# Optimization experiments

Measured on AMD Instinct MI355X. Metric: run time of the kernel, lower is better.

Reference implementation:

```python
import jax, jax.numpy as jnp
import numpy as np

N, E, D_IN, D_H, D_OUT = 100000, 1600000, 128, 128, 47
BN_EPS = 1e-5


def setup_inputs() -> dict:
    key = jax.random.key(0)
    ks = jax.random.split(key, 12)
    x = jax.random.normal(ks[0], (N, D_IN), dtype=jnp.float32)
    edge_index = jax.random.randint(ks[1], (2, E), 0, N, dtype=jnp.int64)
    s = 1.0 / np.sqrt(D_H)
    return {
        "x": x,
        "edge_index": edge_index,
        "W1": jax.random.normal(ks[2], (D_IN, D_H), dtype=jnp.float32) * s,
        "b1": jnp.zeros((D_H,), dtype=jnp.float32),
        "gamma": jax.random.uniform(ks[3], (D_H,), dtype=jnp.float32, minval=0.5, maxval=1.5),
        "beta": jax.random.normal(ks[4], (D_H,), dtype=jnp.float32) * 0.1,
        "mean": jax.random.normal(ks[5], (D_H,), dtype=jnp.float32) * 0.1,
        "var": jax.random.uniform(ks[6], (D_H,), dtype=jnp.float32, minval=0.5, maxval=1.5),
        "W2": jax.random.normal(ks[7], (D_H, D_H), dtype=jnp.float32) * s,
        "b2": jnp.zeros((D_H,), dtype=jnp.float32),
        "Wf": jax.random.normal(ks[8], (D_H, D_OUT), dtype=jnp.float32) * s,
        "bf": jnp.zeros((D_OUT,), dtype=jnp.float32),
    }


def gcn_conv(x, src, dst, W, b, n):
    # x' = x @ W, then symmetric-normalized aggregation with self-loops (PyG GCNConv).
    h = x @ W
    loops = jnp.arange(n, dtype=src.dtype)
    s = jnp.concatenate([src, loops])
    d = jnp.concatenate([dst, loops])
    deg = jax.ops.segment_sum(jnp.ones_like(d, dtype=h.dtype), d, num_segments=n)
    dinv = jnp.where(deg > 0, jax.lax.rsqrt(deg), 0.0)
    norm = dinv[s] * dinv[d]                      # [E+N]
    msg = h[s] * norm[:, None]                    # [E+N, D] gather
    out = jax.ops.segment_sum(msg, d, num_segments=n)  # scatter-add
    return out + b


def reference(x, edge_index, W1, b1, gamma, beta, mean, var, W2, b2, Wf, bf):
    n = x.shape[0]
    src, dst = edge_index[0], edge_index[1]
    # layer 1: GCNConv -> BatchNorm (eval) -> ReLU -> dropout (identity in eval)
    h1 = gcn_conv(x, src, dst, W1, b1, n)
    h1 = (h1 - mean) * jax.lax.rsqrt(var + BN_EPS) * gamma + beta
    h1 = jax.nn.relu(h1)
    # layer 2 (last conv, no BN/act)
    h2 = gcn_conv(h1, src, dst, W2, b2, n)
    # JumpingKnowledge max over layer outputs
    jk = jnp.maximum(h1, h2)
    logits = jk @ Wf + bf
    return jax.nn.log_softmax(logits, axis=1)
```

## Files before the change

kernel.cpp:

```cpp
#include <hip/hip_runtime.h>
#include <math.h>

#define DH 128
#define DOUT 47
#define BN_EPS 1e-5f

typedef __attribute__((ext_vector_type(8))) short short8;
typedef __attribute__((ext_vector_type(4))) float float4v;

__device__ __forceinline__ unsigned bf16_rne(float f) {
    unsigned u = __float_as_uint(f);
    return (u + 0x7fffu + ((u >> 16) & 1u)) >> 16;
}
__device__ __forceinline__ unsigned pack_bf2(float a, float b) {
    return (bf16_rne(a) & 0xffffu) | (bf16_rne(b) << 16);
}
__device__ __forceinline__ float2 unpack_bf2(unsigned u) {
    return make_float2(__uint_as_float(u << 16),
                       __uint_as_float(u & 0xffff0000u));
}


__global__ void zero_int_k(int* __restrict__ p, int n) {
    int i = blockIdx.x * 256 + threadIdx.x;
    if (i < n) p[i] = 0;
}

__global__ __launch_bounds__(256) void scan1_k(const int* __restrict__ counts,
                                               int* __restrict__ offsets,
                                               int* __restrict__ blocksums, int n) {
    __shared__ int sd[256];
    int tid = threadIdx.x;
    int base = blockIdx.x * 1024 + tid * 4;
    int v0 = (base + 0 < n) ? ((counts[base + 0] + 7) & ~7) : 0;
    int v1 = (base + 1 < n) ? ((counts[base + 1] + 7) & ~7) : 0;
    int v2 = (base + 2 < n) ? ((counts[base + 2] + 7) & ~7) : 0;
    int v3 = (base + 3 < n) ? ((counts[base + 3] + 7) & ~7) : 0;
    int tsum = v0 + v1 + v2 + v3;
    sd[tid] = tsum;
    __syncthreads();
    for (int off = 1; off < 256; off <<= 1) {
        int x = (tid >= off) ? sd[tid - off] : 0;
        __syncthreads();
        sd[tid] += x;
        __syncthreads();
    }
    if (tid == 255) blocksums[blockIdx.x] = sd[255];
    int run = sd[tid] - tsum;
    if (base + 0 < n) offsets[base + 0] = run;  run += v0;
    if (base + 1 < n) offsets[base + 1] = run;  run += v1;
    if (base + 2 < n) offsets[base + 2] = run;  run += v2;
    if (base + 3 < n) offsets[base + 3] = run;
}

__global__ __launch_bounds__(128) void scan2_k(int* __restrict__ blocksums, int nb) {
    __shared__ int sd[128];
    int tid = threadIdx.x;
    int v = (tid < nb) ? blocksums[tid] : 0;
    sd[tid] = v;
    __syncthreads();
    for (int off = 1; off < 128; off <<= 1) {
        int x = (tid >= off) ? sd[tid - off] : 0;
        __syncthreads();
        sd[tid] += x;
        __syncthreads();
    }
    if (tid < nb) blocksums[tid] = sd[tid] - v;
}

__global__ void finalize_k(int* __restrict__ offsets, int* __restrict__ cursor,
                           float* __restrict__ dinv, const int* __restrict__ counts,
                           const int* __restrict__ blocksums,
                           int2* __restrict__ ew, int n) {
    int i = blockIdx.x * 256 + threadIdx.x;
    if (i >= n) return;
    int o = offsets[i] + blocksums[i >> 10];
    offsets[i] = o;
    cursor[i] = o;
    int c = counts[i];
    dinv[i] = rsqrtf((float)(c + 1));
    int cP = (c + 7) & ~7;
    int2 z; z.x = 0; z.y = 0;
    for (int j = o + c; j < o + cP; ++j) ew[j] = z;
}

__global__ void fill_k(const int* __restrict__ src, const int* __restrict__ dst,
                       const float* __restrict__ dinv, int* __restrict__ cursor,
                       int2* __restrict__ ew, int e, int n) {
    int i = blockIdx.x * 256 + threadIdx.x;
    int stride = gridDim.x * 256;
    for (; i < e; i += stride) {
        int d = dst[i];
        if ((unsigned)d < (unsigned)n) {
            int s = src[i];
            int pos = atomicAdd(&cursor[d], 1);
            int2 rec;
            rec.x = s;
            rec.y = __float_as_int(dinv[s] * dinv[d]);
            ew[pos] = rec;
        }
    }
}

__global__ __launch_bounds__(256) void wprep_k(const float* __restrict__ W1,
                                               const float* __restrict__ W2,
                                               unsigned* __restrict__ W1b,
                                               unsigned* __restrict__ W2b) {
    const float* W = blockIdx.x ? W2 : W1;
    unsigned* Wb = blockIdx.x ? W2b : W1b;
    int tid = threadIdx.x;
    for (int p = tid; p < 128 * 32; p += 256) {
        int n = p >> 5;
        int k0 = (p & 31) << 2;
        float f0 = W[(size_t)(k0 + 0) * 128 + n];
        float f1 = W[(size_t)(k0 + 1) * 128 + n];
        float f2 = W[(size_t)(k0 + 2) * 128 + n];
        float f3 = W[(size_t)(k0 + 3) * 128 + n];
        uint2 v;
        v.x = pack_bf2(f0, f1);
        v.y = pack_bf2(f2, f3);
        *(uint2*)(Wb + (size_t)n * 64 + (k0 >> 1)) = v;
    }
}

#define COUNT_BLOCKS 2048

__device__ __forceinline__ void gemm_mfma_body(const float* __restrict__ A,
                                               const unsigned* __restrict__ Wb,
                                               unsigned* __restrict__ Cb, int M,
                                               int blk) {
    __shared__ ushort Bl[128 * 136];
    int tid = threadIdx.x;
    {
        unsigned* Bu = (unsigned*)Bl;
        for (int q = tid; q < 128 * 16; q += 256) {
            int row = q >> 4;
            int c = (q & 15) << 2;
            uint4 v = *(const uint4*)(Wb + (size_t)row * 64 + c);
            *(uint4*)(Bu + (size_t)row * 68 + c) = v;
        }
    }
    __syncthreads();

    int lane = tid & 63;
    int wv = tid >> 6;
    int quad = lane >> 4;
    int l15 = lane & 15;
    int r0 = blk * 64 + wv * 16;
    int mload = r0 + l15;
    if (mload > M - 1) mload = M - 1;
    const float* Ar = A + (size_t)mload * 128 + quad * 8;

    float4v acc[8];
#pragma unroll
    for (int t = 0; t < 8; t++) acc[t] = (float4v){0.f, 0.f, 0.f, 0.f};

    for (int kp = 0; kp < 4; ++kp) {
        float4 a0 = *(const float4*)(Ar + kp * 32);
        float4 a1 = *(const float4*)(Ar + kp * 32 + 4);
        float af[8] = {a0.x, a0.y, a0.z, a0.w, a1.x, a1.y, a1.z, a1.w};
        short8 hi, lo;
#pragma unroll
        for (int j = 0; j < 8; j++) {
            unsigned h = bf16_rne(af[j]);
            hi[j] = (short)h;
            float res = af[j] - __uint_as_float(h << 16);
            lo[j] = (short)bf16_rne(res);
        }
        int kb = kp * 32 + quad * 8;
#pragma unroll
        for (int nt = 0; nt < 8; nt++) {
            short8 b8 = *(const short8*)(&Bl[(size_t)(nt * 16 + l15) * 136 + kb]);
            acc[nt] = __builtin_amdgcn_mfma_f32_16x16x32_bf16(hi, b8, acc[nt], 0, 0, 0);
            acc[nt] = __builtin_amdgcn_mfma_f32_16x16x32_bf16(lo, b8, acc[nt], 0, 0, 0);
        }
    }

    ushort* Cu = (ushort*)Cb;
#pragma unroll
    for (int r = 0; r < 4; r++) {
        int row = r0 + quad * 4 + r;
        if (row < M) {
#pragma unroll
            for (int nt = 0; nt < 8; nt++) {
                Cu[(size_t)row * 128 + nt * 16 + l15] = (ushort)bf16_rne(acc[nt][r]);
            }
        }
    }
}

__global__ __launch_bounds__(256) void gemm_mfma_k(const float* __restrict__ A,
                                                   const unsigned* __restrict__ Wb,
                                                   unsigned* __restrict__ Cb, int M) {
    gemm_mfma_body(A, Wb, Cb, M, blockIdx.x);
}

__global__ __launch_bounds__(256) void gemm1_count_k(
    const float* __restrict__ A, const unsigned* __restrict__ Wb,
    unsigned* __restrict__ Cb, int M, int gemmBlocks,
    const int* __restrict__ dst, int* __restrict__ counts, int e, int n) {
    if ((int)blockIdx.x >= gemmBlocks) {
        int bid = blockIdx.x - gemmBlocks;
        int i = bid * 256 + threadIdx.x;
        int stride = COUNT_BLOCKS * 256;
        for (; i < e; i += stride) {
            int d = dst[i];
            if ((unsigned)d < (unsigned)n) atomicAdd(&counts[d], 1);
        }
        return;
    }
    gemm_mfma_body(A, Wb, Cb, M, blockIdx.x);
}

__device__ __forceinline__ float4 agg_core(const uint2* __restrict__ Hu2,
                                           const int2* __restrict__ ew,
                                           int start, int cnt, int node,
                                           int li, int half, float di) {
    float4 acc = make_float4(0.f, 0.f, 0.f, 0.f);
    int groups = ((cnt + 7) & ~7) >> 3;
    if (groups > 0) {
        const int2* p = ew + start + half;
        int2 r[4];
#pragma unroll
        for (int k = 0; k < 4; k++) r[k] = p[2 * k];
        for (int g = 0; g < groups; ++g) {
            uint2 gb[4];
#pragma unroll
            for (int k = 0; k < 4; k++)
                gb[k] = Hu2[(size_t)r[k].x * 32 + li];
            int2 rn[4];
            const int2* pn = p + 8 * (g + 1);
#pragma unroll
            for (int k = 0; k < 4; k++) rn[k] = pn[2 * k];
#pragma unroll
            for (int k = 0; k < 4; k++) {
                float w = __int_as_float(r[k].y);
                float2 f0 = unpack_bf2(gb[k].x);
                float2 f1 = unpack_bf2(gb[k].y);
                acc.x = fmaf(f0.x, w, acc.x);
                acc.y = fmaf(f0.y, w, acc.y);
                acc.z = fmaf(f1.x, w, acc.z);
                acc.w = fmaf(f1.y, w, acc.w);
            }
#pragma unroll
            for (int k = 0; k < 4; k++) r[k] = rn[k];
        }
    }
    acc.x += __shfl_xor(acc.x, 32);
    acc.y += __shfl_xor(acc.y, 32);
    acc.z += __shfl_xor(acc.z, 32);
    acc.w += __shfl_xor(acc.w, 32);
    uint2 sv = Hu2[(size_t)node * 32 + li];
    float ws = di * di;
    float2 s0 = unpack_bf2(sv.x);
    float2 s1 = unpack_bf2(sv.y);
    acc.x = fmaf(s0.x, ws, acc.x);
    acc.y = fmaf(s0.y, ws, acc.y);
    acc.z = fmaf(s1.x, ws, acc.z);
    acc.w = fmaf(s1.y, ws, acc.w);
    return acc;
}

__global__ __launch_bounds__(256) void agg1_k(
    const unsigned* __restrict__ H, const int2* __restrict__ ew,
    const int* __restrict__ offsets, const int* __restrict__ counts,
    const float* __restrict__ dinv, const float* __restrict__ b1,
    const float* __restrict__ gamma, const float* __restrict__ beta,
    const float* __restrict__ mean, const float* __restrict__ var,
    float* __restrict__ H1, int n) {
    int lane = threadIdx.x & 63;
    int li = lane & 31;
    int half = lane >> 5;
    int node = blockIdx.x * 4 + (threadIdx.x >> 6);
    if (node >= n) return;
    float4 acc = agg_core((const uint2*)H, ew, offsets[node], counts[node],
                          node, li, half, dinv[node]);
    if (half == 0) {
        int f0 = li * 4;
        float4 bb = *(const float4*)(b1 + f0);
        float4 mm = *(const float4*)(mean + f0);
        float4 vv = *(const float4*)(var + f0);
        float4 gg = *(const float4*)(gamma + f0);
        float4 be = *(const float4*)(beta + f0);
        float4 o;
        o.x = fmaxf((acc.x + bb.x - mm.x) * rsqrtf(vv.x + BN_EPS) * gg.x + be.x, 0.f);
        o.y = fmaxf((acc.y + bb.y - mm.y) * rsqrtf(vv.y + BN_EPS) * gg.y + be.y, 0.f);
        o.z = fmaxf((acc.z + bb.z - mm.z) * rsqrtf(vv.z + BN_EPS) * gg.z + be.z, 0.f);
        o.w = fmaxf((acc.w + bb.w - mm.w) * rsqrtf(vv.w + BN_EPS) * gg.w + be.w, 0.f);
        *(float4*)(H1 + (size_t)node * 128 + f0) = o;
    }
}

__global__ __launch_bounds__(256) void agg2_k(
    const unsigned* __restrict__ H, const int2* __restrict__ ew,
    const int* __restrict__ offsets, const int* __restrict__ counts,
    const float* __restrict__ dinv, const float* __restrict__ b2,
    float* __restrict__ H1JK, int n) {
    int lane = threadIdx.x & 63;
    int li = lane & 31;
    int half = lane >> 5;
    int node = blockIdx.x * 4 + (threadIdx.x >> 6);
    if (node >= n) return;
    float4 acc = agg_core((const uint2*)H, ew, offsets[node], counts[node],
                          node, li, half, dinv[node]);
    if (half == 0) {
        int f0 = li * 4;
        float4 bb = *(const float4*)(b2 + f0);
        float4* p = (float4*)(H1JK + (size_t)node * 128 + f0);
        float4 h1v = *p;
        float4 o;
        o.x = fmaxf(h1v.x, acc.x + bb.x);
        o.y = fmaxf(h1v.y, acc.y + bb.y);
        o.z = fmaxf(h1v.z, acc.z + bb.z);
        o.w = fmaxf(h1v.w, acc.w + bb.w);
        *p = o;
    }
}

__global__ __launch_bounds__(256) void head_k(const float* __restrict__ JK,
                                              const float* __restrict__ Wf,
                                              const float* __restrict__ bf,
                                              float* __restrict__ out, int n) {
    __shared__ __align__(16) float Bs[48 * 132];
    __shared__ __align__(16) float As[64 * 36];
    int tid = threadIdx.x;
    for (int p = tid; p < 47 * 32; p += 256) {
        int c = p >> 5;
        int k0 = (p & 31) << 2;
        float4 v;
        v.x = Wf[(size_t)(k0 + 0) * DOUT + c];
        v.y = Wf[(size_t)(k0 + 1) * DOUT + c];
        v.z = Wf[(size_t)(k0 + 2) * DOUT + c];
        v.w = Wf[(size_t)(k0 + 3) * DOUT + c];
        *(float4*)(&Bs[c * 132 + k0]) = v;
    }
    int tx = tid & 15;
    int ty = tid >> 4;
    int node0 = blockIdx.x * 64;

    float acc[4][3];
#pragma unroll
    for (int i = 0; i < 4; i++)
#pragma unroll
        for (int j = 0; j < 3; j++) acc[i][j] = 0.f;

    for (int kk = 0; kk < 128; kk += 32) {
        __syncthreads();
        for (int l = tid; l < 512; l += 256) {
            int r = l >> 3;
            int c4 = (l & 7) << 2;
            int row = node0 + r;
            float4 v = make_float4(0.f, 0.f, 0.f, 0.f);
            if (row < n) v = *(const float4*)(JK + (size_t)row * 128 + kk + c4);
            *(float4*)(&As[r * 36 + c4]) = v;
        }
        __syncthreads();
#pragma unroll
        for (int k4 = 0; k4 < 32; k4 += 4) {
            float4 a0 = *(const float4*)(&As[(ty * 4 + 0) * 36 + k4]);
            float4 a1 = *(const float4*)(&As[(ty * 4 + 1) * 36 + k4]);
            float4 a2 = *(const float4*)(&As[(ty * 4 + 2) * 36 + k4]);
            float4 a3 = *(const float4*)(&As[(ty * 4 + 3) * 36 + k4]);
            float4 b0 = *(const float4*)(&Bs[(tx * 3 + 0) * 132 + kk + k4]);
            float4 b1 = *(const float4*)(&Bs[(tx * 3 + 1) * 132 + kk + k4]);
            float4 b2 = *(const float4*)(&Bs[(tx * 3 + 2) * 132 + kk + k4]);
#define DOT_ROW(i, a)                                                        \
            acc[i][0] = fmaf(a.x, b0.x, acc[i][0]);                          \
            acc[i][0] = fmaf(a.y, b0.y, acc[i][0]);                          \
            acc[i][0] = fmaf(a.z, b0.z, acc[i][0]);                          \
            acc[i][0] = fmaf(a.w, b0.w, acc[i][0]);                          \
            acc[i][1] = fmaf(a.x, b1.x, acc[i][1]);                          \
            acc[i][1] = fmaf(a.y, b1.y, acc[i][1]);                          \
            acc[i][1] = fmaf(a.z, b1.z, acc[i][1]);                          \
            acc[i][1] = fmaf(a.w, b1.w, acc[i][1]);                          \
            acc[i][2] = fmaf(a.x, b2.x, acc[i][2]);                          \
            acc[i][2] = fmaf(a.y, b2.y, acc[i][2]);                          \
            acc[i][2] = fmaf(a.z, b2.z, acc[i][2]);                          \
            acc[i][2] = fmaf(a.w, b2.w, acc[i][2]);
            DOT_ROW(0, a0)
            DOT_ROW(1, a1)
            DOT_ROW(2, a2)
            DOT_ROW(3, a3)
#undef DOT_ROW
        }
    }

    float bfv[3];
#pragma unroll
    for (int j = 0; j < 3; j++) {
        int c = tx * 3 + j;
        bfv[j] = (c < DOUT) ? bf[c] : 0.f;
    }
#pragma unroll
    for (int i = 0; i < 4; i++) {
        int node = node0 + ty * 4 + i;
        float l0 = acc[i][0] + bfv[0];
        float l1 = acc[i][1] + bfv[1];
        float l2 = acc[i][2] + bfv[2];
        bool v2ok = (tx * 3 + 2) < DOUT;
        float m = fmaxf(l0, l1);
        if (v2ok) m = fmaxf(m, l2);
        for (int off = 8; off >= 1; off >>= 1) m = fmaxf(m, __shfl_xor(m, off));
        float s = expf(l0 - m) + expf(l1 - m) + (v2ok ? expf(l2 - m) : 0.f);
        for (int off = 8; off >= 1; off >>= 1) s += __shfl_xor(s, off);
        float ls = m + logf(s);
        if (node < n) {
            float* o = out + (size_t)node * DOUT + tx * 3;
            o[0] = l0 - ls;
            o[1] = l1 - ls;
            if (v2ok) o[2] = l2 - ls;
        }
    }
}

extern "C" void kernel_launch(void* const* d_in, const int* in_sizes, int n_in,
                              void* d_out, int out_size, void* d_ws, size_t ws_size,
                              hipStream_t stream) {
    const float* x     = (const float*)d_in[0];
    const int*   ei    = (const int*)d_in[1];
    const float* W1    = (const float*)d_in[2];
    const float* b1    = (const float*)d_in[3];
    const float* gamma = (const float*)d_in[4];
    const float* beta  = (const float*)d_in[5];
    const float* mean  = (const float*)d_in[6];
    const float* var   = (const float*)d_in[7];
    const float* W2    = (const float*)d_in[8];
    const float* b2    = (const float*)d_in[9];
    const float* Wf    = (const float*)d_in[10];
    const float* bf    = (const float*)d_in[11];
    float* out = (float*)d_out;

    int N_ = in_sizes[0] / 128;
    int E_ = in_sizes[1] / 2;
    const int* src = ei;
    const int* dst = ei + E_;

    char* ws = (char*)d_ws;
    unsigned* bufA = (unsigned*)ws; ws += (size_t)N_ * 64 * 4;
    float* h1      = (float*)ws;  ws += (size_t)N_ * 128 * 4;
    int*   counts  = (int*)ws;    ws += (size_t)N_ * 4;
    int*   offsets = (int*)ws;    ws += (size_t)N_ * 4;
    int*   cursor  = (int*)ws;    ws += (size_t)N_ * 4;
    float* dinv    = (float*)ws;  ws += (size_t)N_ * 4;
    int2*  ew      = (int2*)ws;   ws += ((size_t)E_ + 7 * (size_t)N_ + 64) * 8;
    int*   bsums   = (int*)ws;    ws += 1024 * 4;
    unsigned* W1b  = (unsigned*)ws; ws += 128 * 64 * 4;
    unsigned* W2b  = (unsigned*)ws; ws += 128 * 64 * 4;

    int nb = (N_ + 1023) / 1024;
    int gemmBlocks = (N_ + 63) / 64;

    zero_int_k<<<(N_ + 255) / 256, 256, 0, stream>>>(counts, N_);
    wprep_k<<<2, 256, 0, stream>>>(W1, W2, W1b, W2b);
    gemm1_count_k<<<gemmBlocks + COUNT_BLOCKS, 256, 0, stream>>>(
        x, W1b, bufA, N_, gemmBlocks, dst, counts, E_, N_);
    scan1_k<<<nb, 256, 0, stream>>>(counts, offsets, bsums, N_);
    scan2_k<<<1, 128, 0, stream>>>(bsums, nb);
    finalize_k<<<(N_ + 255) / 256, 256, 0, stream>>>(offsets, cursor, dinv,
                                                     counts, bsums, ew, N_);
    fill_k<<<2048, 256, 0, stream>>>(src, dst, dinv, cursor, ew, E_, N_);

    agg1_k<<<(N_ + 3) / 4, 256, 0, stream>>>(bufA, ew, offsets, counts, dinv,
                                             b1, gamma, beta, mean, var, h1, N_);
    gemm_mfma_k<<<gemmBlocks, 256, 0, stream>>>(h1, W2b, bufA, N_);
    agg2_k<<<(N_ + 3) / 4, 256, 0, stream>>>(bufA, ew, offsets, counts, dinv,
                                             b2, h1, N_);
    head_k<<<(N_ + 63) / 64, 256, 0, stream>>>(h1, Wf, bf, out, N_);
}
```

Measured before the change: 507.6 us.

## Overlap layer-1 GEMM with CSR fill instead of degree count; vectorize edge loops

Moves the edge degree counting into its own standalone kernel, and has the first GEMM share a launch with the CSR fill step instead. Both edge kernels now read four edge indices per thread with int4 loads and issue batched atomics, rather than using grid-stride scalar loops. The aim is to hide the costlier fill stage behind the GEMM and cut per-edge instruction and load overhead. It also drops the bounds check on destination indices.

```diff
diff --git a/kernel.cpp b/kernel.cpp
--- a/kernel.cpp
+++ b/kernel.cpp
@@ -24,6 +24,21 @@
 __global__ void zero_int_k(int* __restrict__ p, int n) {
     int i = blockIdx.x * 256 + threadIdx.x;
     if (i < n) p[i] = 0;
+}
+
+__global__ __launch_bounds__(256) void count4_k(const int* __restrict__ dst,
+                                                int* __restrict__ counts,
+                                                int e, int n) {
+    int i0 = (blockIdx.x * 256 + threadIdx.x) * 4;
+    if (i0 + 4 <= e) {
+        int4 d4 = *(const int4*)(dst + i0);
+        atomicAdd(&counts[d4.x], 1);
+        atomicAdd(&counts[d4.y], 1);
+        atomicAdd(&counts[d4.z], 1);
+        atomicAdd(&counts[d4.w], 1);
+    } else {
+        for (int i = i0; i < e; i++) atomicAdd(&counts[dst[i]], 1);
+    }
 }
 
 __global__ __launch_bounds__(256) void scan1_k(const int* __restrict__ counts,
@@ -84,20 +99,34 @@
     for (int j = o + c; j < o + cP; ++j) ew[j] = z;
 }
 
-__global__ void fill_k(const int* __restrict__ src, const int* __restrict__ dst,
-                       const float* __restrict__ dinv, int* __restrict__ cursor,
-                       int2* __restrict__ ew, int e, int n) {
-    int i = blockIdx.x * 256 + threadIdx.x;
-    int stride = gridDim.x * 256;
-    for (; i < e; i += stride) {
-        int d = dst[i];
-        if ((unsigned)d < (unsigned)n) {
-            int s = src[i];
+__device__ __forceinline__ void fill4_body(const int* __restrict__ src,
+                                           const int* __restrict__ dst,
+                                           const float* __restrict__ dinv,
+                                           int* __restrict__ cursor,
+                                           int2* __restrict__ ew, int e, int bid) {
+    int i0 = (bid * 256 + threadIdx.x) * 4;
+    if (i0 + 4 <= e) {
+        int4 s4 = *(const int4*)(src + i0);
+        int4 d4 = *(const int4*)(dst + i0);
+        int sa[4] = {s4.x, s4.y, s4.z, s4.w};
+        int da[4] = {d4.x, d4.y, d4.z, d4.w};
+        float w[4];
+#pragma unroll
+        for (int k = 0; k < 4; k++) w[k] = dinv[sa[k]] * dinv[da[k]];
+        int p[4];
+#pragma unroll
+        for (int k = 0; k < 4; k++) p[k] = atomicAdd(&cursor[da[k]], 1);
+#pragma unroll
+        for (int k = 0; k < 4; k++) {
+            int2 r; r.x = sa[k]; r.y = __float_as_int(w[k]);
+            ew[p[k]] = r;
+        }
+    } else {
+        for (int i = i0; i < e; i++) {
+            int s = src[i], d = dst[i];
             int pos = atomicAdd(&cursor[d], 1);
-            int2 rec;
-            rec.x = s;
-            rec.y = __float_as_int(dinv[s] * dinv[d]);
-            ew[pos] = rec;
+            int2 r; r.x = s; r.y = __float_as_int(dinv[s] * dinv[d]);
+            ew[pos] = r;
         }
     }
 }
@@ -123,8 +152,6 @@
     }
 }
 
-#define COUNT_BLOCKS 2048
-
 __device__ __forceinline__ void gemm_mfma_body(const float* __restrict__ A,
                                                const unsigned* __restrict__ Wb,
                                                unsigned* __restrict__ Cb, int M,
@@ -195,18 +222,14 @@
     gemm_mfma_body(A, Wb, Cb, M, blockIdx.x);
 }
 
-__global__ __launch_bounds__(256) void gemm1_count_k(
+__global__ __launch_bounds__(256) void gemm1_fill_k(
     const float* __restrict__ A, const unsigned* __restrict__ Wb,
     unsigned* __restrict__ Cb, int M, int gemmBlocks,
-    const int* __restrict__ dst, int* __restrict__ counts, int e, int n) {
+    const int* __restrict__ src, const int* __restrict__ dst,
+    const float* __restrict__ dinv, int* __restrict__ cursor,
+    int2* __restrict__ ew, int e) {
     if ((int)blockIdx.x >= gemmBlocks) {
-        int bid = blockIdx.x - gemmBlocks;
-        int i = bid * 256 + threadIdx.x;
-        int stride = COUNT_BLOCKS * 256;
-        for (; i < e; i += stride) {
-            int d = dst[i];
-            if ((unsigned)d < (unsigned)n) atomicAdd(&counts[d], 1);
-        }
+        fill4_body(src, dst, dinv, cursor, ew, e, blockIdx.x - gemmBlocks);
         return;
     }
     gemm_mfma_body(A, Wb, Cb, M, blockIdx.x);
@@ -449,16 +472,17 @@
 
     int nb = (N_ + 1023) / 1024;
     int gemmBlocks = (N_ + 63) / 64;
+    int edgeBlocks = (E_ + 1023) / 1024;
 
     zero_int_k<<<(N_ + 255) / 256, 256, 0, stream>>>(counts, N_);
     wprep_k<<<2, 256, 0, stream>>>(W1, W2, W1b, W2b);
-    gemm1_count_k<<<gemmBlocks + COUNT_BLOCKS, 256, 0, stream>>>(
-        x, W1b, bufA, N_, gemmBlocks, dst, counts, E_, N_);
+    count4_k<<<edgeBlocks, 256, 0, stream>>>(dst, counts, E_, N_);
     scan1_k<<<nb, 256, 0, stream>>>(counts, offsets, bsums, N_);
     scan2_k<<<1, 128, 0, stream>>>(bsums, nb);
     finalize_k<<<(N_ + 255) / 256, 256, 0, stream>>>(offsets, cursor, dinv,
                                                      counts, bsums, ew, N_);
-    fill_k<<<2048, 256, 0, stream>>>(src, dst, dinv, cursor, ew, E_, N_);
+    gemm1_fill_k<<<gemmBlocks + edgeBlocks, 256, 0, stream>>>(
+        x, W1b, bufA, N_, gemmBlocks, src, dst, dinv, cursor, ew, E_);
 
     agg1_k<<<(N_ + 3) / 4, 256, 0, stream>>>(bufA, ew, offsets, counts, dinv,
                                              b1, gamma, beta, mean, var, h1, N_);
```

After: 547.6 us. +7.9%, slower.
